# Kernel optimization log

Measured on AMD Instinct MI355X. Metric: run time of the kernel, lower is better.

The kernel has to match this reference:

```python
import jax, jax.numpy as jnp
import numpy as np

NEG_SLOPE = 0.2
NUM_NODES = 100000
NUM_EDGES = 200000
NNZ = 1600000
IN_C = 128
OUT_C = 128
STAR = 64


def setup_inputs() -> dict:
    key = jax.random.key(0)
    ks = jax.random.split(key, 12)
    X = jax.random.normal(ks[0], (NUM_NODES, IN_C), dtype=jnp.float32)
    V = jax.random.randint(ks[1], (NNZ,), 0, NUM_NODES)
    E = jax.random.randint(ks[2], (NNZ,), 0, NUM_EDGES)
    S_features = jax.random.normal(ks[3], (NUM_EDGES, STAR), dtype=jnp.float32)
    s = 1.0 / np.sqrt(IN_C)
    Wx = jax.random.uniform(ks[4], (IN_C, OUT_C), minval=-s, maxval=s)
    bx = jax.random.uniform(ks[5], (OUT_C,), minval=-s, maxval=s)
    Wv = jax.random.uniform(ks[6], (IN_C, OUT_C), minval=-s, maxval=s)
    bv = jax.random.uniform(ks[7], (OUT_C,), minval=-s, maxval=s)
    sa = 1.0 / np.sqrt(OUT_C)
    a_vec = jax.random.uniform(ks[8], (OUT_C,), minval=-sa, maxval=sa)
    st = 1.0 / np.sqrt(OUT_C + STAR)
    Wt = jax.random.uniform(ks[9], (OUT_C + STAR, OUT_C), minval=-st, maxval=st)
    bt = jax.random.uniform(ks[10], (OUT_C,), minval=-st, maxval=st)
    return {"X": X, "V": V, "E": E, "S_features": S_features,
            "Wx": Wx, "bx": bx, "Wv": Wv, "bv": bv,
            "a_vec": a_vec, "Wt": Wt, "bt": bt}


def _segment_softmax(s, seg, num_segments):
    m = jax.ops.segment_max(s, seg, num_segments=num_segments)
    e = jnp.exp(s - m[seg])
    denom = jax.ops.segment_sum(e, seg, num_segments=num_segments)
    return e / denom[seg]


def reference(X, V, E, S_features, Wx, bx, Wv, bv, a_vec, Wt, bt):
    # DPHGNNConv forward (eval mode: dropout = identity)
    X_init = X @ Wx + bx                      # [N, out]
    X_feat = X @ Wv + bv                      # [N, out]
    scores = X_feat @ a_vec                   # [N]
    s = jax.nn.leaky_relu(scores[V], NEG_SLOPE)  # [nnz]
    w = _segment_softmax(s, E, NUM_EDGES)     # [nnz]
    Xev = X_feat[V] * w[:, None]              # [nnz, out]
    Y_v2e = jax.ops.segment_sum(Xev, E, num_segments=NUM_EDGES)
    Y_v2e = jax.nn.elu(Y_v2e)
    e_msg = jnp.concatenate([Y_v2e, S_features], axis=1)  # [E, out+star]
    Y = e_msg @ Wt + bt                       # [E, out]
    Yev = Y[E]                                # [nnz, out]
    num = jax.ops.segment_sum(Yev, V, num_segments=NUM_NODES)
    cnt = jax.ops.segment_sum(jnp.ones((NNZ,), jnp.float32), V, num_segments=NUM_NODES)
    Xn = num / jnp.maximum(cnt, 1.0)[:, None]  # scatter_mean
    Xn = jax.nn.elu(Xn)                        # is_last=False
    return Xn + X_init
```

## Files before the change

kernel.cpp:

```cpp
#include <hip/hip_runtime.h>
#include <math.h>

#define N_NODES 100000
#define N_EDGES 200000
#define NNZ_    1600000
#define INC  128
#define OUTC 128
#define STAR_ 64
#define NEG 0.2f
#define NBIN_E 391
#define NBIN_V 196
#define NBIN (NBIN_E + NBIN_V)
#define CHUNK 4000
#define CAP_E 5120
#define CAP_V 9216
#define PAIR_SZ (NBIN_E*CAP_E + NBIN_V*CAP_V)
#define CAPI 288
#define CAPN 448

typedef __attribute__((ext_vector_type(8))) short bf16x8_t;
typedef __attribute__((ext_vector_type(8))) unsigned short u16x8;
typedef __attribute__((ext_vector_type(4))) float f32x4_t;

__device__ __forceinline__ float leaky(float x){ return x > 0.f ? x : NEG*x; }
__device__ __forceinline__ float elu1(float x){ return x > 0.f ? x : __expf(x)-1.f; }
__device__ __forceinline__ unsigned short f2bf(float f){
  unsigned u = __float_as_uint(f);
  unsigned r = u + 0x7FFFu + ((u >> 16) & 1u);
  return (unsigned short)(r >> 16);
}
__device__ __forceinline__ float bf2f(unsigned short h){
  return __uint_as_float(((unsigned)h) << 16);
}
__device__ __forceinline__ int padBaseD(int bin){
  return bin < NBIN_E ? bin*CAP_E : NBIN_E*CAP_E + (bin-NBIN_E)*CAP_V;
}

__global__ void k_cvt(const float* __restrict__ Wx, const float* __restrict__ Wv,
                      const float* __restrict__ Wt,
                      unsigned short* __restrict__ WcatT, unsigned short* __restrict__ WtT,
                      int* __restrict__ binCur){
  const int i = blockIdx.x*256 + threadIdx.x;
  if (i < 256*128){
    const int n = i >> 7, k = i & 127;
    const float v = (n < 128) ? Wx[k*128 + n] : Wv[k*128 + (n-128)];
    WcatT[n*128 + k] = f2bf(v);
  }
  const int j = i - 256*128;
  if (j >= 0 && j < 128*192){
    const int n = j / 192, k = j - n*192;
    WtT[n*192 + k] = f2bf(Wt[k*128 + n]);
  }
  if (blockIdx.x == 0){
    for (int p = threadIdx.x; p < NBIN; p += 256) binCur[p] = padBaseD(p);
  }
}

__global__ __launch_bounds__(256) void k_gemm1(const float* __restrict__ X,
    const unsigned short* __restrict__ WcatT,
    const float* __restrict__ bx, const float* __restrict__ bv,
    const float* __restrict__ av,
    float* __restrict__ Xinit, unsigned short* __restrict__ Xfb,
    float* __restrict__ scores){
  __shared__ unsigned short xb[16][136];
  __shared__ float sc[16];
  const int tid = threadIdx.x;
  const int lane = tid & 63, w = tid >> 6;
  const int quad = lane >> 4, l16 = lane & 15;
  const int r0 = blockIdx.x * 16;
  if (tid < 16) sc[tid] = 0.f;
  {
    const int r = tid >> 4;
    const int c0 = (tid & 15) * 8;
    const float4 a4 = *(const float4*)&X[(size_t)(r0+r)*INC + c0];
    const float4 b4 = *(const float4*)&X[(size_t)(r0+r)*INC + c0 + 4];
    bf16x8_t pk;
    pk[0]=(short)f2bf(a4.x); pk[1]=(short)f2bf(a4.y); pk[2]=(short)f2bf(a4.z); pk[3]=(short)f2bf(a4.w);
    pk[4]=(short)f2bf(b4.x); pk[5]=(short)f2bf(b4.y); pk[6]=(short)f2bf(b4.z); pk[7]=(short)f2bf(b4.w);
    *(bf16x8_t*)&xb[r][c0] = pk;
  }
  __syncthreads();
  f32x4_t acc[4] = {{0,0,0,0},{0,0,0,0},{0,0,0,0},{0,0,0,0}};
  const int n_base = w*64 + l16;
  for (int s = 0; s < 4; ++s){
    const bf16x8_t af = *(const bf16x8_t*)&xb[l16][s*32 + quad*8];
    #pragma unroll
    for (int nt = 0; nt < 4; ++nt){
      const int n = n_base + nt*16;
      const bf16x8_t bf = *(const bf16x8_t*)&WcatT[(size_t)n*128 + s*32 + quad*8];
      acc[nt] = __builtin_amdgcn_mfma_f32_16x16x32_bf16(af, bf, acc[nt], 0, 0, 0);
    }
  }
  float pr[4] = {0.f, 0.f, 0.f, 0.f};
  #pragma unroll
  for (int nt = 0; nt < 4; ++nt){
    const int n = n_base + nt*16;
    const float bias = (n < 128) ? bx[n] : bv[n-128];
    #pragma unroll
    for (int r = 0; r < 4; ++r){
      const int m = quad*4 + r;
      const float val = acc[nt][r] + bias;
      if (n < 128) Xinit[(size_t)(r0+m)*OUTC + n] = val;
      else {
        Xfb[(size_t)(r0+m)*OUTC + (n-128)] = f2bf(val);
        pr[r] += val * av[n-128];
      }
    }
  }
  if (w >= 2){
    #pragma unroll
    for (int r = 0; r < 4; ++r) atomicAdd(&sc[quad*4 + r], pr[r]);
  }
  __syncthreads();
  if (tid < 16) scores[r0 + tid] = sc[tid];
}


__global__ __launch_bounds__(256) void k_binA(const int* __restrict__ V, const int* __restrict__ E,
                                              int* __restrict__ binCur, int2* __restrict__ pair){
  __shared__ int h[NBIN];
  __shared__ int base[NBIN];
  for (int p = threadIdx.x; p < NBIN; p += 256) h[p] = 0;
  __syncthreads();
  const int start = blockIdx.x*CHUNK, end = start + CHUNK;
  for (int i = start + threadIdx.x; i < end; i += 256){
    atomicAdd(&h[E[i] >> 9], 1);
    atomicAdd(&h[NBIN_E + (V[i] >> 9)], 1);
  }
  __syncthreads();
  for (int p = threadIdx.x; p < NBIN; p += 256)
    base[p] = h[p] ? atomicAdd(&binCur[p], h[p]) : 0;
  __syncthreads();
  for (int p = threadIdx.x; p < NBIN; p += 256) h[p] = 0;
  __syncthreads();
  for (int i = start + threadIdx.x; i < end; i += 256){
    const int e = E[i], v = V[i];
    const int be = e >> 9, bv = NBIN_E + (v >> 9);
    const int se = base[be] + atomicAdd(&h[be], 1);
    const int sv = base[bv] + atomicAdd(&h[bv], 1);
    pair[se] = make_int2(e, v);
    pair[sv] = make_int2(v, e);
  }
}

__global__ __launch_bounds__(1024) void k_binscan(const int* __restrict__ binCur,
                                                  int* __restrict__ binBase, int* __restrict__ binCnt,
                                                  int2* __restrict__ vw, int* __restrict__ eIdxV){
  __shared__ int s[1024];
  const int tid = threadIdx.x;
  const int v = (tid < NBIN) ? (binCur[tid] - padBaseD(tid)) : 0;
  s[tid] = v; __syncthreads();
  for (int o = 1; o < 1024; o <<= 1){
    const int u = (tid >= o) ? s[tid-o] : 0;
    __syncthreads();
    s[tid] += u;
    __syncthreads();
  }
  if (tid < NBIN){ binBase[tid] = s[tid] - v; binCnt[tid] = v; }
  if (tid < 16){ vw[NNZ_ + tid] = make_int2(0, 0); eIdxV[NNZ_ + tid] = 0; }
}

__global__ __launch_bounds__(256) void k_binB(const int2* __restrict__ pair,
    const int* __restrict__ binBase, const int* __restrict__ binCnt,
    const float* __restrict__ scores,
    int2* __restrict__ vw, int* __restrict__ eIdxV,
    int* __restrict__ cntE, int* __restrict__ startsE,
    int* __restrict__ cntV, int* __restrict__ startsV,
    float* __restrict__ dens){
  __shared__ int h[512], sc0[512], sc1[512];
  __shared__ float dsh[512];
  const int bin = blockIdx.x;
  const bool isE = bin < NBIN_E;
  const int nb = isE ? bin : bin - NBIN_E;
  const int bucket0 = nb << 9;
  const int nBuckTot = isE ? N_EDGES : N_NODES;
  const int pstart = padBaseD(bin);
  const int n = binCnt[bin];
  const int itemBase = isE ? binBase[bin] : binBase[bin] - NNZ_;
  const int tid = threadIdx.x;
  for (int p = tid; p < 512; p += 256){ h[p] = 0; dsh[p] = 0.f; }
  __syncthreads();
  for (int j = tid; j < n; j += 256) atomicAdd(&h[pair[pstart + j].x & 511], 1);
  __syncthreads();
  for (int p = tid; p < 512; p += 256) sc0[p] = h[p];
  __syncthreads();
  int* a = sc0; int* b = sc1;
  for (int o = 1; o < 512; o <<= 1){
    for (int p = tid; p < 512; p += 256) b[p] = a[p] + (p >= o ? a[p-o] : 0);
    __syncthreads();
    int* t = a; a = b; b = t;
  }
  for (int p = tid; p < 512; p += 256){
    const int excl = a[p] - h[p];
    b[p] = itemBase + excl;
    const int bucket = bucket0 + p;
    if (bucket < nBuckTot){
      if (isE){ cntE[bucket] = h[p]; startsE[bucket] = itemBase + excl; }
      else    { cntV[bucket] = h[p]; startsV[bucket] = itemBase + excl; }
    }
  }
  __syncthreads();
  for (int j = tid; j < n; j += 256){
    const int2 kv = pair[pstart + j];
    const int slot = atomicAdd(&b[kv.x & 511], 1);
    if (isE){
      const float ex = __expf(leaky(scores[kv.y]));
      vw[slot] = make_int2(kv.y, __float_as_int(ex));
      atomicAdd(&dsh[kv.x & 511], ex);
    } else {
      eIdxV[slot] = kv.y;
    }
  }
  __syncthreads();
  if (isE){
    for (int p = tid; p < 512; p += 256){
      const int bucket = bucket0 + p;
      if (bucket < N_EDGES) dens[bucket] = dsh[p];
    }
  }
}

__global__ __launch_bounds__(256) void k_edge(
    const int* __restrict__ cntE, const int* __restrict__ startsE,
    const int2* __restrict__ vw, const float* __restrict__ dens,
    const unsigned short* __restrict__ Xfb,
    const float* __restrict__ S, const unsigned short* __restrict__ WtT,
    const float* __restrict__ bt, unsigned short* __restrict__ Ybf) {
  __shared__ int2 inc[CAPI + 8];
  __shared__ unsigned short msg[16][200];
  const int tid = threadIdx.x;
  const int lane = tid & 63, w = tid >> 6;
  const int e0 = blockIdx.x * 16;
  const int g16 = tid >> 4, s16 = tid & 15;

  const int st0 = startsE[e0];
  const int lim = startsE[e0 + 15] + cntE[e0 + 15] - st0;

  for (int i = tid; i < CAPI + 8; i += 256)
    inc[i] = (i < lim) ? vw[st0 + i] : make_int2(0, 0);

  {
    const float4 s4 = *(const float4*)&S[(size_t)(e0+g16)*STAR_ + s16*4];
    ushort4 pk; pk.x=f2bf(s4.x); pk.y=f2bf(s4.y); pk.z=f2bf(s4.z); pk.w=f2bf(s4.w);
    *(ushort4*)&msg[g16][128 + s16*4] = pk;
  }
  __syncthreads();

  const int e = e0 + g16;
  const int deg = cntE[e];
  const int lo  = startsE[e] - st0;
  const int c8 = s16 * 8;
  float ac[8] = {0.f,0.f,0.f,0.f,0.f,0.f,0.f,0.f};
  if (lo + deg <= CAPI) {
    for (int j = 0; j < deg; j += 8) {
      int2 pp[8];
      #pragma unroll
      for (int k = 0; k < 8; ++k) pp[k] = inc[lo + j + k];
      u16x8 xx[8];
      #pragma unroll
      for (int k = 0; k < 8; ++k)
        xx[k] = *(const u16x8*)&Xfb[(size_t)pp[k].x*OUTC + c8];
      #pragma unroll
      for (int k = 0; k < 8; ++k) {
        const float wgt = (j + k < deg) ? __int_as_float(pp[k].y) : 0.f;
        #pragma unroll
        for (int q = 0; q < 8; ++q) ac[q] += wgt * bf2f(xx[k][q]);
      }
    }
  } else {
    const int st = st0 + lo;
    for (int j = 0; j < deg; j += 8) {
      int2 pp[8];
      #pragma unroll
      for (int k = 0; k < 8; ++k) pp[k] = vw[st + j + k];
      u16x8 xx[8];
      #pragma unroll
      for (int k = 0; k < 8; ++k)
        xx[k] = *(const u16x8*)&Xfb[(size_t)pp[k].x*OUTC + c8];
      #pragma unroll
      for (int k = 0; k < 8; ++k) {
        const float wgt = (j + k < deg) ? __int_as_float(pp[k].y) : 0.f;
        #pragma unroll
        for (int q = 0; q < 8; ++q) ac[q] += wgt * bf2f(xx[k][q]);
      }
    }
  }
  {
    const float invd = deg > 0 ? 1.f/dens[e] : 0.f;
    u16x8 pk;
    #pragma unroll
    for (int q = 0; q < 8; ++q) pk[q] = f2bf(elu1(ac[q]*invd));
    *(u16x8*)&msg[g16][c8] = pk;
  }
  __syncthreads();

  const int quad = lane >> 4, l16 = lane & 15;
  f32x4_t acc0 = {0,0,0,0}, acc1 = {0,0,0,0};
  const int n0 = w * 32;
  for (int s = 0; s < 6; ++s) {
    const bf16x8_t af = *(const bf16x8_t*)&msg[l16][s*32 + quad*8];
    const bf16x8_t b0 = *(const bf16x8_t*)&WtT[(size_t)(n0 + l16)*192      + s*32 + quad*8];
    const bf16x8_t b1 = *(const bf16x8_t*)&WtT[(size_t)(n0 + 16 + l16)*192 + s*32 + quad*8];
    acc0 = __builtin_amdgcn_mfma_f32_16x16x32_bf16(af, b0, acc0, 0, 0, 0);
    acc1 = __builtin_amdgcn_mfma_f32_16x16x32_bf16(af, b1, acc1, 0, 0, 0);
  }
  const float bt0 = bt[n0 + l16], bt1 = bt[n0 + 16 + l16];
  #pragma unroll
  for (int r = 0; r < 4; ++r) {
    const int m = quad*4 + r;
    Ybf[(size_t)(e0+m)*OUTC + n0 + l16]      = f2bf(acc0[r] + bt0);
    Ybf[(size_t)(e0+m)*OUTC + n0 + 16 + l16] = f2bf(acc1[r] + bt1);
  }
}

__global__ __launch_bounds__(256) void k_node(
    const int* __restrict__ cntV, const int* __restrict__ startsV,
    const int* __restrict__ eIdxV,
    const unsigned short* __restrict__ Ybf, float* __restrict__ out) {
  __shared__ int elds[CAPN + 8];
  const int tid = threadIdx.x;
  const int g16 = tid >> 4, s16 = tid & 15;
  const int v0 = blockIdx.x * 16;

  const int st0 = startsV[v0];
  const int lim = startsV[v0 + 15] + cntV[v0 + 15] - st0;
  for (int i = tid; i < CAPN + 8; i += 256)
    elds[i] = (i < lim) ? eIdxV[st0 + i] : 0;
  __syncthreads();

  const int v = v0 + g16;
  const int deg = cntV[v];
  const int lo  = startsV[v] - st0;
  const int c8 = s16 * 8;
  float ac[8] = {0.f,0.f,0.f,0.f,0.f,0.f,0.f,0.f};
  if (lo + deg <= CAPN) {
    for (int j = 0; j < deg; j += 8) {
      int ee[8];
      #pragma unroll
      for (int k = 0; k < 8; ++k) ee[k] = elds[lo + j + k];
      u16x8 yy[8];
      #pragma unroll
      for (int k = 0; k < 8; ++k)
        yy[k] = *(const u16x8*)&Ybf[(size_t)ee[k]*OUTC + c8];
      #pragma unroll
      for (int k = 0; k < 8; ++k) {
        const float pz = (j + k < deg) ? 1.f : 0.f;
        #pragma unroll
        for (int q = 0; q < 8; ++q) ac[q] += pz * bf2f(yy[k][q]);
      }
    }
  } else {
    const int st = st0 + lo;
    for (int j = 0; j < deg; j += 8) {
      int ee[8];
      #pragma unroll
      for (int k = 0; k < 8; ++k) ee[k] = eIdxV[st + j + k];
      u16x8 yy[8];
      #pragma unroll
      for (int k = 0; k < 8; ++k)
        yy[k] = *(const u16x8*)&Ybf[(size_t)ee[k]*OUTC + c8];
      #pragma unroll
      for (int k = 0; k < 8; ++k) {
        const float pz = (j + k < deg) ? 1.f : 0.f;
        #pragma unroll
        for (int q = 0; q < 8; ++q) ac[q] += pz * bf2f(yy[k][q]);
      }
    }
  }
  const float invd = 1.f / fmaxf((float)deg, 1.f);
  float4 o0 = *(float4*)&out[(size_t)v*OUTC + c8];
  float4 o1 = *(float4*)&out[(size_t)v*OUTC + c8 + 4];
  o0.x = elu1(ac[0]*invd) + o0.x;
  o0.y = elu1(ac[1]*invd) + o0.y;
  o0.z = elu1(ac[2]*invd) + o0.z;
  o0.w = elu1(ac[3]*invd) + o0.w;
  o1.x = elu1(ac[4]*invd) + o1.x;
  o1.y = elu1(ac[5]*invd) + o1.y;
  o1.z = elu1(ac[6]*invd) + o1.z;
  o1.w = elu1(ac[7]*invd) + o1.w;
  *(float4*)&out[(size_t)v*OUTC + c8]     = o0;
  *(float4*)&out[(size_t)v*OUTC + c8 + 4] = o1;
}

extern "C" void kernel_launch(void* const* d_in, const int* in_sizes, int n_in,
                              void* d_out, int out_size, void* d_ws, size_t ws_size,
                              hipStream_t stream) {
  const float* X  = (const float*)d_in[0];
  const int*   V  = (const int*)d_in[1];
  const int*   E  = (const int*)d_in[2];
  const float* S  = (const float*)d_in[3];
  const float* Wx = (const float*)d_in[4];
  const float* bx = (const float*)d_in[5];
  const float* Wv = (const float*)d_in[6];
  const float* bv = (const float*)d_in[7];
  const float* av = (const float*)d_in[8];
  const float* Wt = (const float*)d_in[9];
  const float* bt = (const float*)d_in[10];
  float* out = (float*)d_out;

  char* ws = (char*)d_ws;
  size_t off = 0;
  auto alloc = [&](size_t bytes) -> void* {
    off = (off + 255) & ~(size_t)255;
    void* p = ws + off; off += bytes; return p;
  };
  unsigned short* Xfb   = (unsigned short*)alloc((size_t)N_NODES*OUTC*2);
  unsigned short* Ybf   = (unsigned short*)alloc((size_t)N_EDGES*OUTC*2);
  float* scores = (float*)alloc((size_t)N_NODES*4);
  unsigned short* WcatT = (unsigned short*)alloc((size_t)256*128*2);
  unsigned short* WtT   = (unsigned short*)alloc((size_t)128*192*2);
  int2* pair   = (int2*)alloc((size_t)PAIR_SZ*8);
  int* binBase = (int*)alloc((size_t)NBIN*4);
  int* binCur  = (int*)alloc((size_t)NBIN*4);
  int* binCnt  = (int*)alloc((size_t)NBIN*4);
  int* cntE    = (int*)alloc((size_t)N_EDGES*4);
  int* cntV    = (int*)alloc((size_t)N_NODES*4);
  int* startsE = (int*)alloc((size_t)N_EDGES*4);
  int* startsV = (int*)alloc((size_t)N_NODES*4);
  int2* vw     = (int2*)alloc((size_t)(NNZ_+16)*8);
  int* eIdxV   = (int*)alloc((size_t)(NNZ_+16)*4);
  float* dens  = (float*)alloc((size_t)N_EDGES*4);

  k_cvt<<<(256*128 + 128*192 + 255)/256, 256, 0, stream>>>(Wx, Wv, Wt, WcatT, WtT, binCur);
  k_gemm1<<<N_NODES/16, 256, 0, stream>>>(X, WcatT, bx, bv, av, out, Xfb, scores);

  k_binA<<<NNZ_/CHUNK, 256, 0, stream>>>(V, E, binCur, pair);
  k_binscan<<<1, 1024, 0, stream>>>(binCur, binBase, binCnt, vw, eIdxV);
  k_binB<<<NBIN, 256, 0, stream>>>(pair, binBase, binCnt, scores, vw, eIdxV,
                                   cntE, startsE, cntV, startsV, dens);

  k_edge<<<N_EDGES/16, 256, 0, stream>>>(cntE, startsE, vw, dens, Xfb, S, WtT, bt, Ybf);
  k_node<<<N_NODES/16, 256, 0, stream>>>(cntV, startsV, eIdxV, Ybf, out);
}
```

Measured before the change: 513.4 us.

## Fuse binning into GEMM launch, widen binB blocks, halve nodes per k_node block

Merges the k_binA binning pass into the first GEMM kernel as extra blocks, so the independent binning and node-projection work share one launch and can overlap on the GPU. k_binB now runs 512 threads so each thread owns exactly one bucket, which removes the strided loops. k_node processes 8 nodes per block with 32 lanes per node, each lane handling 4 channels instead of 8, giving more blocks and more parallel gathers. The cost is a larger shared-memory footprint in the fused kernel and narrower loads per lane in k_node.

```diff
diff --git a/kernel.cpp b/kernel.cpp
--- a/kernel.cpp
+++ b/kernel.cpp
@@ -12,11 +12,12 @@
 #define NBIN_V 196
 #define NBIN (NBIN_E + NBIN_V)
 #define CHUNK 4000
+#define NBLK_A (NNZ_/CHUNK)
 #define CAP_E 5120
 #define CAP_V 9216
 #define PAIR_SZ (NBIN_E*CAP_E + NBIN_V*CAP_V)
 #define CAPI 288
-#define CAPN 448
+#define CAPN 288
 
 typedef __attribute__((ext_vector_type(8))) short bf16x8_t;
 typedef __attribute__((ext_vector_type(8))) unsigned short u16x8;
@@ -56,18 +57,48 @@
   }
 }
 
-__global__ __launch_bounds__(256) void k_gemm1(const float* __restrict__ X,
-    const unsigned short* __restrict__ WcatT,
+__global__ __launch_bounds__(256) void k_front(
+    const float* __restrict__ X, const unsigned short* __restrict__ WcatT,
     const float* __restrict__ bx, const float* __restrict__ bv,
     const float* __restrict__ av,
     float* __restrict__ Xinit, unsigned short* __restrict__ Xfb,
-    float* __restrict__ scores){
+    float* __restrict__ scores,
+    const int* __restrict__ V, const int* __restrict__ E,
+    int* __restrict__ binCur, int2* __restrict__ pair){
+  __shared__ int hA[NBIN];
+  __shared__ int baseA[NBIN];
   __shared__ unsigned short xb[16][136];
   __shared__ float sc[16];
   const int tid = threadIdx.x;
+
+  if (blockIdx.x < NBLK_A) {
+    for (int p = tid; p < NBIN; p += 256) hA[p] = 0;
+    __syncthreads();
+    const int start = blockIdx.x*CHUNK, end = start + CHUNK;
+    for (int i = start + tid; i < end; i += 256){
+      atomicAdd(&hA[E[i] >> 9], 1);
+      atomicAdd(&hA[NBIN_E + (V[i] >> 9)], 1);
+    }
+    __syncthreads();
+    for (int p = tid; p < NBIN; p += 256)
+      baseA[p] = hA[p] ? atomicAdd(&binCur[p], hA[p]) : 0;
+    __syncthreads();
+    for (int p = tid; p < NBIN; p += 256) hA[p] = 0;
+    __syncthreads();
+    for (int i = start + tid; i < end; i += 256){
+      const int e = E[i], v = V[i];
+      const int be = e >> 9, bv_ = NBIN_E + (v >> 9);
+      const int se = baseA[be]  + atomicAdd(&hA[be],  1);
+      const int sv = baseA[bv_] + atomicAdd(&hA[bv_], 1);
+      pair[se] = make_int2(e, v);
+      pair[sv] = make_int2(v, e);
+    }
+    return;
+  }
+
   const int lane = tid & 63, w = tid >> 6;
   const int quad = lane >> 4, l16 = lane & 15;
-  const int r0 = blockIdx.x * 16;
+  const int r0 = (blockIdx.x - NBLK_A) * 16;
   if (tid < 16) sc[tid] = 0.f;
   {
     const int r = tid >> 4;
@@ -115,34 +146,6 @@
   if (tid < 16) scores[r0 + tid] = sc[tid];
 }
 
-
-__global__ __launch_bounds__(256) void k_binA(const int* __restrict__ V, const int* __restrict__ E,
-                                              int* __restrict__ binCur, int2* __restrict__ pair){
-  __shared__ int h[NBIN];
-  __shared__ int base[NBIN];
-  for (int p = threadIdx.x; p < NBIN; p += 256) h[p] = 0;
-  __syncthreads();
-  const int start = blockIdx.x*CHUNK, end = start + CHUNK;
-  for (int i = start + threadIdx.x; i < end; i += 256){
-    atomicAdd(&h[E[i] >> 9], 1);
-    atomicAdd(&h[NBIN_E + (V[i] >> 9)], 1);
-  }
-  __syncthreads();
-  for (int p = threadIdx.x; p < NBIN; p += 256)
-    base[p] = h[p] ? atomicAdd(&binCur[p], h[p]) : 0;
-  __syncthreads();
-  for (int p = threadIdx.x; p < NBIN; p += 256) h[p] = 0;
-  __syncthreads();
-  for (int i = start + threadIdx.x; i < end; i += 256){
-    const int e = E[i], v = V[i];
-    const int be = e >> 9, bv = NBIN_E + (v >> 9);
-    const int se = base[be] + atomicAdd(&h[be], 1);
-    const int sv = base[bv] + atomicAdd(&h[bv], 1);
-    pair[se] = make_int2(e, v);
-    pair[sv] = make_int2(v, e);
-  }
-}
-
 __global__ __launch_bounds__(1024) void k_binscan(const int* __restrict__ binCur,
                                                   int* __restrict__ binBase, int* __restrict__ binCnt,
                                                   int2* __restrict__ vw, int* __restrict__ eIdxV){
@@ -160,7 +163,7 @@
   if (tid < 16){ vw[NNZ_ + tid] = make_int2(0, 0); eIdxV[NNZ_ + tid] = 0; }
 }
 
-__global__ __launch_bounds__(256) void k_binB(const int2* __restrict__ pair,
+__global__ __launch_bounds__(512) void k_binB(const int2* __restrict__ pair,
     const int* __restrict__ binBase, const int* __restrict__ binCnt,
     const float* __restrict__ scores,
     int2* __restrict__ vw, int* __restrict__ eIdxV,
@@ -178,29 +181,29 @@
   const int n = binCnt[bin];
   const int itemBase = isE ? binBase[bin] : binBase[bin] - NNZ_;
   const int tid = threadIdx.x;
-  for (int p = tid; p < 512; p += 256){ h[p] = 0; dsh[p] = 0.f; }
-  __syncthreads();
-  for (int j = tid; j < n; j += 256) atomicAdd(&h[pair[pstart + j].x & 511], 1);
-  __syncthreads();
-  for (int p = tid; p < 512; p += 256) sc0[p] = h[p];
+  h[tid] = 0; dsh[tid] = 0.f;
+  __syncthreads();
+  for (int j = tid; j < n; j += 512) atomicAdd(&h[pair[pstart + j].x & 511], 1);
+  __syncthreads();
+  sc0[tid] = h[tid];
   __syncthreads();
   int* a = sc0; int* b = sc1;
   for (int o = 1; o < 512; o <<= 1){
-    for (int p = tid; p < 512; p += 256) b[p] = a[p] + (p >= o ? a[p-o] : 0);
+    b[tid] = a[tid] + (tid >= o ? a[tid-o] : 0);
     __syncthreads();
     int* t = a; a = b; b = t;
   }
-  for (int p = tid; p < 512; p += 256){
-    const int excl = a[p] - h[p];
-    b[p] = itemBase + excl;
-    const int bucket = bucket0 + p;
+  {
+    const int excl = a[tid] - h[tid];
+    b[tid] = itemBase + excl;
+    const int bucket = bucket0 + tid;
     if (bucket < nBuckTot){
-      if (isE){ cntE[bucket] = h[p]; startsE[bucket] = itemBase + excl; }
-      else    { cntV[bucket] = h[p]; startsV[bucket] = itemBase + excl; }
-    }
-  }
-  __syncthreads();
-  for (int j = tid; j < n; j += 256){
+      if (isE){ cntE[bucket] = h[tid]; startsE[bucket] = itemBase + excl; }
+      else    { cntV[bucket] = h[tid]; startsV[bucket] = itemBase + excl; }
+    }
+  }
+  __syncthreads();
+  for (int j = tid; j < n; j += 512){
     const int2 kv = pair[pstart + j];
     const int slot = atomicAdd(&b[kv.x & 511], 1);
     if (isE){
@@ -213,10 +216,8 @@
   }
   __syncthreads();
   if (isE){
-    for (int p = tid; p < 512; p += 256){
-      const int bucket = bucket0 + p;
-      if (bucket < N_EDGES) dens[bucket] = dsh[p];
-    }
+    const int bucket = bucket0 + tid;
+    if (bucket < N_EDGES) dens[bucket] = dsh[tid];
   }
 }
 
@@ -319,34 +320,34 @@
     const unsigned short* __restrict__ Ybf, float* __restrict__ out) {
   __shared__ int elds[CAPN + 8];
   const int tid = threadIdx.x;
-  const int g16 = tid >> 4, s16 = tid & 15;
-  const int v0 = blockIdx.x * 16;
+  const int sub = tid & 31, grp = tid >> 5;
+  const int v0 = blockIdx.x * 8;
 
   const int st0 = startsV[v0];
-  const int lim = startsV[v0 + 15] + cntV[v0 + 15] - st0;
+  const int lim = startsV[v0 + 7] + cntV[v0 + 7] - st0;
   for (int i = tid; i < CAPN + 8; i += 256)
     elds[i] = (i < lim) ? eIdxV[st0 + i] : 0;
   __syncthreads();
 
-  const int v = v0 + g16;
+  const int v = v0 + grp;
+  const int c4 = sub * 4;
   const int deg = cntV[v];
   const int lo  = startsV[v] - st0;
-  const int c8 = s16 * 8;
-  float ac[8] = {0.f,0.f,0.f,0.f,0.f,0.f,0.f,0.f};
+  float a0=0.f, a1=0.f, a2=0.f, a3=0.f;
   if (lo + deg <= CAPN) {
     for (int j = 0; j < deg; j += 8) {
       int ee[8];
       #pragma unroll
       for (int k = 0; k < 8; ++k) ee[k] = elds[lo + j + k];
-      u16x8 yy[8];
+      ushort4 yy[8];
       #pragma unroll
       for (int k = 0; k < 8; ++k)
-        yy[k] = *(const u16x8*)&Ybf[(size_t)ee[k]*OUTC + c8];
+        yy[k] = *(const ushort4*)&Ybf[(size_t)ee[k]*OUTC + c4];
       #pragma unroll
       for (int k = 0; k < 8; ++k) {
         const float pz = (j + k < deg) ? 1.f : 0.f;
-        #pragma unroll
-        for (int q = 0; q < 8; ++q) ac[q] += pz * bf2f(yy[k][q]);
+        a0 += pz * bf2f(yy[k].x); a1 += pz * bf2f(yy[k].y);
+        a2 += pz * bf2f(yy[k].z); a3 += pz * bf2f(yy[k].w);
       }
     }
   } else {
@@ -355,31 +356,25 @@
       int ee[8];
       #pragma unroll
       for (int k = 0; k < 8; ++k) ee[k] = eIdxV[st + j + k];
-      u16x8 yy[8];
+      ushort4 yy[8];
       #pragma unroll
       for (int k = 0; k < 8; ++k)
-        yy[k] = *(const u16x8*)&Ybf[(size_t)ee[k]*OUTC + c8];
+        yy[k] = *(const ushort4*)&Ybf[(size_t)ee[k]*OUTC + c4];
       #pragma unroll
       for (int k = 0; k < 8; ++k) {
         const float pz = (j + k < deg) ? 1.f : 0.f;
-        #pragma unroll
-        for (int q = 0; q < 8; ++q) ac[q] += pz * bf2f(yy[k][q]);
+        a0 += pz * bf2f(yy[k].x); a1 += pz * bf2f(yy[k].y);
+        a2 += pz * bf2f(yy[k].z); a3 += pz * bf2f(yy[k].w);
       }
     }
   }
   const float invd = 1.f / fmaxf((float)deg, 1.f);
-  float4 o0 = *(float4*)&out[(size_t)v*OUTC + c8];
-  float4 o1 = *(float4*)&out[(size_t)v*OUTC + c8 + 4];
-  o0.x = elu1(ac[0]*invd) + o0.x;
-  o0.y = elu1(ac[1]*invd) + o0.y;
-  o0.z = elu1(ac[2]*invd) + o0.z;
-  o0.w = elu1(ac[3]*invd) + o0.w;
-  o1.x = elu1(ac[4]*invd) + o1.x;
-  o1.y = elu1(ac[5]*invd) + o1.y;
-  o1.z = elu1(ac[6]*invd) + o1.z;
-  o1.w = elu1(ac[7]*invd) + o1.w;
-  *(float4*)&out[(size_t)v*OUTC + c8]     = o0;
-  *(float4*)&out[(size_t)v*OUTC + c8 + 4] = o1;
+  float4 o = *(float4*)&out[(size_t)v*OUTC + c4];
+  o.x = elu1(a0*invd) + o.x;
+  o.y = elu1(a1*invd) + o.y;
+  o.z = elu1(a2*invd) + o.z;
+  o.w = elu1(a3*invd) + o.w;
+  *(float4*)&out[(size_t)v*OUTC + c4] = o;
 }
 
 extern "C" void kernel_launch(void* const* d_in, const int* in_sizes, int n_in,
@@ -422,13 +417,12 @@
   float* dens  = (float*)alloc((size_t)N_EDGES*4);
 
   k_cvt<<<(256*128 + 128*192 + 255)/256, 256, 0, stream>>>(Wx, Wv, Wt, WcatT, WtT, binCur);
-  k_gemm1<<<N_NODES/16, 256, 0, stream>>>(X, WcatT, bx, bv, av, out, Xfb, scores);
-
-  k_binA<<<NNZ_/CHUNK, 256, 0, stream>>>(V, E, binCur, pair);
+  k_front<<<NBLK_A + N_NODES/16, 256, 0, stream>>>(X, WcatT, bx, bv, av, out, Xfb, scores,
+                                                   V, E, binCur, pair);
   k_binscan<<<1, 1024, 0, stream>>>(binCur, binBase, binCnt, vw, eIdxV);
-  k_binB<<<NBIN, 256, 0, stream>>>(pair, binBase, binCnt, scores, vw, eIdxV,
+  k_binB<<<NBIN, 512, 0, stream>>>(pair, binBase, binCnt, scores, vw, eIdxV,
                                    cntE, startsE, cntV, startsV, dens);
 
   k_edge<<<N_EDGES/16, 256, 0, stream>>>(cntE, startsE, vw, dens, Xfb, S, WtT, bt, Ybf);
-  k_node<<<N_NODES/16, 256, 0, stream>>>(cntV, startsV, eIdxV, Ybf, out);
-}
+  k_node<<<N_NODES/8, 256, 0, stream>>>(cntV, startsV, eIdxV, Ybf, out);
+}
```

After: 473.7 us. 1.08x faster.
